# Kernel optimization log

Measured on AMD Instinct MI355X. Metric: run time of the kernel, lower is better.

The kernel has to match this reference:

```python
import jax, jax.numpy as jnp
import numpy as np

DIM = 192
TDIM = 192
HEADS = 6
WS = (2, 7, 7)
SS = (1, 3, 3)
MLP_HID = 4 * DIM
RANK = DIM // 8
EPS = 1e-6


def _rel_pos_index(ws):
    wd, wh, ww = ws
    coords = np.stack(np.meshgrid(np.arange(wd), np.arange(wh), np.arange(ww), indexing='ij'))
    cf = coords.reshape(3, -1)
    rel = (cf[:, :, None] - cf[:, None, :]).transpose(1, 2, 0).astype(np.int64)
    rel[..., 0] += wd - 1
    rel[..., 1] += wh - 1
    rel[..., 2] += ww - 1
    rel[..., 0] *= (2 * wh - 1) * (2 * ww - 1)
    rel[..., 1] *= (2 * ww - 1)
    return rel.sum(-1)  # (N, N)


def _window_partition(x, ws):
    B, D, H, W, C = x.shape
    x = x.reshape(B, D // ws[0], ws[0], H // ws[1], ws[1], W // ws[2], ws[2], C)
    return x.transpose(0, 1, 3, 5, 2, 4, 6, 7).reshape(-1, ws[0] * ws[1] * ws[2], C)


def _window_reverse(w, ws, B, D, H, W):
    x = w.reshape(B, D // ws[0], H // ws[1], W // ws[2], ws[0], ws[1], ws[2], -1)
    return x.transpose(0, 1, 4, 2, 5, 3, 6, 7).reshape(B, D, H, W, -1)


def _ln(x):
    m = x.mean(-1, keepdims=True)
    v = ((x - m) ** 2).mean(-1, keepdims=True)
    return (x - m) * jax.lax.rsqrt(v + EPS)


def _compute_mask_np(Dp, Hp, Wp, ws, ss):
    img = np.zeros((1, Dp, Hp, Wp, 1), dtype=np.float32)
    cnt = 0
    for d in (slice(0, -ws[0]), slice(-ws[0], -ss[0]), slice(-ss[0], None)):
        for h in (slice(0, -ws[1]), slice(-ws[1], -ss[1]), slice(-ss[1], None)):
            for w in (slice(0, -ws[2]), slice(-ws[2], -ss[2]), slice(-ss[2], None)):
                img[:, d, h, w, :] = cnt
                cnt += 1
    x = img.reshape(1, Dp // ws[0], ws[0], Hp // ws[1], ws[1], Wp // ws[2], ws[2], 1)
    mw = x.transpose(0, 1, 3, 5, 2, 4, 6, 7).reshape(-1, ws[0] * ws[1] * ws[2])
    am = mw[:, None, :] - mw[:, :, None]
    return np.where(am != 0, np.float32(-100.0), np.float32(0.0))


def setup_inputs() -> dict:
    key = jax.random.key(0)
    ks = jax.random.split(key, 16)
    B, D, H, W, C = 1, 16, 64, 128, DIM
    Dp = D + (-D) % WS[0]
    Hp = H + (-H) % WS[1]
    Wp = W + (-W) % WS[2]
    s = 0.02
    bias_tab = (2 * WS[0] - 1) * (2 * WS[1] - 1) * (2 * WS[2] - 1)
    return {
        'x': jax.random.normal(ks[0], (B, D, H, W, C), jnp.float32),
        'mask_matrix': jnp.asarray(_compute_mask_np(Dp, Hp, Wp, WS, SS)),
        't': jax.random.normal(ks[1], (B, TDIM), jnp.float32),
        'w_qkv': jax.random.normal(ks[2], (C, 3 * C), jnp.float32) * s,
        'b_qkv': jnp.zeros((3 * C,), jnp.float32),
        'rel_bias': jax.random.normal(ks[3], (bias_tab, HEADS), jnp.float32) * s,
        'w_proj': jax.random.normal(ks[4], (C, C), jnp.float32) * s,
        'b_proj': jnp.zeros((C,), jnp.float32),
        'w1': jax.random.normal(ks[5], (C, MLP_HID), jnp.float32) * s,
        'b1': jnp.zeros((MLP_HID,), jnp.float32),
        'w2': jax.random.normal(ks[6], (MLP_HID, C), jnp.float32) * s,
        'b2': jnp.zeros((C,), jnp.float32),
        'wa1': jax.random.normal(ks[7], (TDIM, RANK), jnp.float32) * s,
        'wa2': jax.random.normal(ks[8], (RANK, 6 * C), jnp.float32) * s,
        'ba2': jax.random.normal(ks[9], (6 * C,), jnp.float32) * s,
    }


def reference(x, mask_matrix, t, w_qkv, b_qkv, rel_bias, w_proj, b_proj, w1, b1, w2, b2, wa1, wa2, ba2):
    B, D, H, W, C = x.shape
    hd = C // HEADS
    # AdaLN modulation params
    mod = (jax.nn.silu(t) @ wa1) @ wa2 + ba2  # (B, 6C)
    sh_msa, sc_msa, g_msa, sh_mlp, sc_mlp, g_mlp = jnp.split(mod, 6, axis=1)

    def modulate(y, sh, sc):
        return y * (1 + sc[:, None, None, None, :]) + sh[:, None, None, None, :]

    shortcut = x
    y = modulate(_ln(x), sh_msa, sc_msa)
    # pad to window multiples
    pad_d, pad_h, pad_w = (-D) % WS[0], (-H) % WS[1], (-W) % WS[2]
    y = jnp.pad(y, ((0, 0), (0, pad_d), (0, pad_h), (0, pad_w), (0, 0)))
    Dp, Hp, Wp = D + pad_d, H + pad_h, W + pad_w
    # cyclic shift
    y = jnp.roll(y, (-SS[0], -SS[1], -SS[2]), axis=(1, 2, 3))
    xw = _window_partition(y, WS)  # (B*nW, N, C)
    N = xw.shape[1]
    qkv = (xw @ w_qkv + b_qkv).reshape(-1, N, 3, HEADS, hd)
    q, k, v = qkv[:, :, 0], qkv[:, :, 1], qkv[:, :, 2]
    scale = hd ** -0.5
    attn = jnp.einsum('bnhd,bmhd->bhnm', q * scale, k)  # (B*nW, H, N, N)
    rpi = _rel_pos_index(WS)
    bias = rel_bias[rpi.reshape(-1)].reshape(N, N, HEADS).transpose(2, 0, 1)
    attn = attn + bias[None]
    nW = mask_matrix.shape[0]
    attn = attn.reshape(B, nW, HEADS, N, N) + mask_matrix[None, :, None]
    attn = jax.nn.softmax(attn, axis=-1).reshape(-1, HEADS, N, N)
    out = jnp.einsum('bhnm,bmhd->bnhd', attn, v).reshape(-1, N, C)
    out = out @ w_proj + b_proj
    y = _window_reverse(out, WS, B, Dp, Hp, Wp)
    y = jnp.roll(y, (SS[0], SS[1], SS[2]), axis=(1, 2, 3))
    y = y[:, :D, :H, :W, :]
    x1 = shortcut + g_msa[:, None, None, None, :] * y
    y2 = modulate(_ln(x1), sh_mlp, sc_mlp)
    h = jax.nn.gelu(y2 @ w1 + b1, approximate=False) @ w2 + b2
    return x1 + g_mlp[:, None, None, None, :] * h
```

## Files before the change

### kernel.cpp

```cpp
#include <hip/hip_runtime.h>
#include <hip/hip_bf16.h>

typedef __bf16 bf16x8 __attribute__((ext_vector_type(8)));
typedef float  f32x4  __attribute__((ext_vector_type(4)));
typedef unsigned int u32x4 __attribute__((ext_vector_type(4)));

__device__ inline unsigned short f2bf(float f) {
    union { __hip_bfloat16 h; unsigned short u; } cv;
    cv.h = __float2bfloat16(f);
    return cv.u;
}

__device__ inline bf16x8 load8(const unsigned short* p) {
    uint2 lo = *(const uint2*)(p);
    uint2 hi = *(const uint2*)(p + 16);
    u32x4 v; v[0] = lo.x; v[1] = lo.y; v[2] = hi.x; v[3] = hi.y;
    return __builtin_bit_cast(bf16x8, v);
}

__device__ inline f32x4 mfma16(bf16x8 a, bf16x8 b, f32x4 c) {
    return __builtin_amdgcn_mfma_f32_16x16x32_bf16(a, b, c, 0, 0, 0);
}

__device__ inline bool winmapT(int gg, int& T) {
    int win = gg / 98, n = gg % 98;
    int wdi = win / 190, rem = win % 190, whi = rem / 19, wwi = rem % 19;
    int td = n / 49, th = (n / 7) % 7, tw = n % 7;
    int sd = (wdi * 2 + td + 1) & 15;
    int sh = whi * 7 + th + 3; if (sh >= 70) sh -= 70;
    int sw = wwi * 7 + tw + 3; if (sw >= 133) sw -= 133;
    if (sh < 64 && sw < 128) { T = (sd * 64 + sh) * 128 + sw; return true; }
    return false;
}

__global__ __launch_bounds__(256) void mod_k(const float* __restrict__ t,
    const float* __restrict__ wa1, const float* __restrict__ wa2,
    const float* __restrict__ ba2, float* __restrict__ mod)
{
    __shared__ float st[192];
    __shared__ float a[24];
    int tid = threadIdx.x;
    if (tid < 192) { float x = t[tid]; st[tid] = x / (1.f + __expf(-x)); }
    __syncthreads();
    if (tid < 24) {
        float s = 0.f;
        for (int c = 0; c < 192; ++c) s += st[c] * wa1[c * 24 + tid];
        a[tid] = s;
    }
    __syncthreads();
    for (int j = tid; j < 1152; j += 256) {
        float s = ba2[j];
        for (int r = 0; r < 24; ++r) s += a[r] * wa2[r * 1152 + j];
        mod[j] = s;
    }
}

__global__ __launch_bounds__(256) void prep_k(
    const float* __restrict__ wqkv, const float* __restrict__ wproj,
    const float* __restrict__ w1, const float* __restrict__ w2,
    const float* __restrict__ relb,
    unsigned short* __restrict__ wqkvT, unsigned short* __restrict__ wprojT,
    unsigned short* __restrict__ w1T, unsigned short* __restrict__ w2T,
    float* __restrict__ btab)
{
    int i = blockIdx.x * 256 + threadIdx.x;
    if (i < 110592) { int n = i / 192, k = i % 192; wqkvT[i] = f2bf(wqkv[k * 576 + n]); return; }
    i -= 110592;
    if (i < 36864)  { int n = i / 192, k = i % 192; wprojT[i] = f2bf(wproj[k * 192 + n]); return; }
    i -= 36864;
    if (i < 147456) { int n = i / 192, k = i % 192; w1T[i] = f2bf(w1[k * 768 + n]); return; }
    i -= 147456;
    if (i < 147456) { int n = i / 768, k = i % 768; w2T[i] = f2bf(w2[k * 192 + n]); return; }
    i -= 147456;
    if (i < 461952) {
        int mt = i / 57624, rem = i % 57624;
        int h = rem / 9604, rm2 = rem % 9604;
        int n = rm2 / 98, m = rm2 % 98;
        int tdn = n / 49, thn = (n / 7) % 7, twn = n % 7;
        int tdm = m / 49, thm = (m / 7) % 7, twm = m % 7;
        int idx = (tdn - tdm + 1) * 169 + (thn - thm + 6) * 13 + (twn - twm + 6);
        float b = relb[idx * 6 + h];
        int bd = mt & 1, bh = (mt >> 1) & 1, bw = (mt >> 2) & 1;
        int idn = (bd ? (tdn == 0 ? 1 : 2) : 0) * 9 + (bh ? (thn < 4 ? 1 : 2) : 0) * 3 + (bw ? (twn < 4 ? 1 : 2) : 0);
        int idm = (bd ? (tdm == 0 ? 1 : 2) : 0) * 9 + (bh ? (thm < 4 ? 1 : 2) : 0) * 3 + (bw ? (twm < 4 ? 1 : 2) : 0);
        btab[i] = b + ((idn != idm) ? -100.f : 0.f);
    }
}

__global__ __launch_bounds__(256) void stats_f32_k(const float* __restrict__ x,
    float* __restrict__ st)
{
    int tok = blockIdx.x * 4 + (threadIdx.x >> 6);
    int lane = threadIdx.x & 63;
    const float* p = x + (size_t)tok * 192;
    float a = p[lane], b = p[64 + lane], c = p[128 + lane];
    float s = a + b + c, q = a * a + b * b + c * c;
    for (int m = 32; m; m >>= 1) { s += __shfl_xor(s, m); q += __shfl_xor(q, m); }
    if (lane == 0) {
        float mean = s * (1.f / 192.f);
        float var  = q * (1.f / 192.f) - mean * mean;
        st[2 * tok] = mean;
        st[2 * tok + 1] = rsqrtf(var + 1e-6f);
    }
}

template<int FN, int STAGE, int EPI>
__global__ __launch_bounds__(256) void gemm_k(
    const unsigned short* __restrict__ A, const float* __restrict__ Af,
    const unsigned short* __restrict__ BT, const float* __restrict__ bias,
    unsigned short* __restrict__ outB, float* outF,
    const float* __restrict__ auxF, const float* __restrict__ stats,
    const float* __restrict__ mod, int row0, int M, int N, int K)
{
    constexpr int BN = FN * 32;
    __shared__ unsigned short As[128][44];
    __shared__ unsigned short Bs[BN][44];
    const int t = threadIdx.x;
    const int n0 = blockIdx.x * BN, m0 = blockIdx.y * 128;
    const int lr = t >> 2, lk = (t & 3) * 8;
    const int wid = t >> 6, lane = t & 63;
    const int lg = lane >> 4, l16 = lane & 15;
    const int wm = (wid >> 1) * 64, wn = (wid & 1) * (FN * 16);
    f32x4 acc[4][FN] = {};

    float mn[2] = {0.f, 0.f}, rs[2] = {0.f, 0.f};
    size_t sbase[2] = {0, 0};
    bool va[2] = {false, false};
    #pragma unroll
    for (int rr = 0; rr < 2; ++rr) {
        int g = m0 + lr + rr * 64;
        if (STAGE == 1) {
            int T;
            if (g < M && winmapT(row0 + g, T)) {
                va[rr] = true; sbase[rr] = (size_t)T * 192;
                mn[rr] = stats[2 * T]; rs[rr] = stats[2 * T + 1];
            }
        } else if (STAGE == 2) {
            int tok = row0 + g;
            sbase[rr] = (size_t)tok * 192;
            mn[rr] = stats[2 * tok]; rs[rr] = stats[2 * tok + 1];
        }
    }

    for (int kk = 0; kk < K; kk += 32) {
        #pragma unroll
        for (int rr = 0; rr < 2; ++rr) {
            int r = lr + rr * 64;
            int g = m0 + r;
            uint4 w = make_uint4(0u, 0u, 0u, 0u);
            if (STAGE == 0) {
                if (g < M) w = *(const uint4*)(A + (size_t)g * K + kk + lk);
            } else if (STAGE == 1) {
                if (va[rr]) {
                    float4 xa = *(const float4*)(Af + sbase[rr] + kk + lk);
                    float4 xb = *(const float4*)(Af + sbase[rr] + kk + lk + 4);
                    float xs[8] = {xa.x, xa.y, xa.z, xa.w, xb.x, xb.y, xb.z, xb.w};
                    unsigned short o[8];
                    #pragma unroll
                    for (int j = 0; j < 8; ++j) {
                        int c = kk + lk + j;
                        o[j] = f2bf((xs[j] - mn[rr]) * rs[rr] * (1.f + mod[192 + c]) + mod[c]);
                    }
                    w = make_uint4((unsigned)o[0] | ((unsigned)o[1] << 16), (unsigned)o[2] | ((unsigned)o[3] << 16),
                                   (unsigned)o[4] | ((unsigned)o[5] << 16), (unsigned)o[6] | ((unsigned)o[7] << 16));
                }
            } else {
                float4 xa = *(const float4*)(Af + sbase[rr] + kk + lk);
                float4 xb = *(const float4*)(Af + sbase[rr] + kk + lk + 4);
                float xs[8] = {xa.x, xa.y, xa.z, xa.w, xb.x, xb.y, xb.z, xb.w};
                unsigned short o[8];
                #pragma unroll
                for (int j = 0; j < 8; ++j) {
                    int c = kk + lk + j;
                    o[j] = f2bf((xs[j] - mn[rr]) * rs[rr] * (1.f + mod[768 + c]) + mod[576 + c]);
                }
                w = make_uint4((unsigned)o[0] | ((unsigned)o[1] << 16), (unsigned)o[2] | ((unsigned)o[3] << 16),
                               (unsigned)o[4] | ((unsigned)o[5] << 16), (unsigned)o[6] | ((unsigned)o[7] << 16));
            }
            *(uint2*)(&As[r][lk])     = make_uint2(w.x, w.y);
            *(uint2*)(&As[r][lk + 4]) = make_uint2(w.z, w.w);
        }
        #pragma unroll
        for (int rr = 0; rr < BN / 64; ++rr) {
            int r = lr + rr * 64;
            int gn = n0 + r;
            uint4 w = make_uint4(0u, 0u, 0u, 0u);
            if (gn < N) w = *(const uint4*)(BT + (size_t)gn * K + kk + lk);
            *(uint2*)(&Bs[r][lk])     = make_uint2(w.x, w.y);
            *(uint2*)(&Bs[r][lk + 4]) = make_uint2(w.z, w.w);
        }
        __syncthreads();
        bf16x8 af[4], bv[FN];
        #pragma unroll
        for (int i = 0; i < 4; ++i) af[i] = load8(&As[wm + i * 16 + l16][4 * lg]);
        #pragma unroll
        for (int j = 0; j < FN; ++j) bv[j] = load8(&Bs[wn + j * 16 + l16][4 * lg]);
        #pragma unroll
        for (int i = 0; i < 4; ++i)
        #pragma unroll
        for (int j = 0; j < FN; ++j)
            acc[i][j] = mfma16(af[i], bv[j], acc[i][j]);
        __syncthreads();
    }

    #pragma unroll
    for (int i = 0; i < 4; ++i)
    #pragma unroll
    for (int j = 0; j < FN; ++j) {
        int gcol = n0 + wn + j * 16 + l16;
        if (gcol >= N) continue;
        float b = bias[gcol];
        #pragma unroll
        for (int e = 0; e < 4; ++e) {
            int grow = m0 + wm + i * 16 + lg * 4 + e;
            if (grow >= M) continue;
            float v = acc[i][j][e] + b;
            if (EPI == 0) {
                outB[(size_t)grow * N + gcol] = f2bf(v);
            } else if (EPI == 1) {
                float gl = 0.5f * v * (1.f + erff(v * 0.70710678118654752f));
                outB[(size_t)grow * N + gcol] = f2bf(gl);
            } else if (EPI == 2) {
                int T;
                if (winmapT(row0 + grow, T)) {
                    size_t idx = (size_t)T * 192 + gcol;
                    outF[idx] = auxF[idx] + mod[384 + gcol] * v;
                }
            } else {
                size_t idx = (size_t)(row0 + grow) * 192 + gcol;
                outF[idx] = outF[idx] + mod[960 + gcol] * v;
            }
        }
    }
}

__global__ __launch_bounds__(256) void attn_k(
    const unsigned short* __restrict__ qkv, const float* __restrict__ btab,
    unsigned short* __restrict__ out)
{
    __shared__ __align__(16) char smem[40320];
    unsigned short* Qs  = (unsigned short*)smem;
    unsigned short* Ks  = (unsigned short*)(smem + 9856);
    unsigned short* Pbf = (unsigned short*)smem;
    unsigned short* VT  = (unsigned short*)(smem + 31360);

    const int blk = blockIdx.x;
    const int win = blk / 6, h = blk % 6;
    const int t = threadIdx.x;
    const int wid = t >> 6, lg = (t >> 4) & 3, l16 = t & 15;
    const size_t rb = (size_t)win * 98;

    const int wdi = win / 190, remw = win % 190, whi = remw / 19, wwi = remw % 19;
    const int mt = (wdi == 7 ? 1 : 0) | (whi == 9 ? 2 : 0) | (wwi == 18 ? 4 : 0);
    const float* bt = btab + (size_t)(mt * 6 + h) * 9604;

    for (int i = t; i < 98 * 4; i += 256) {
        int r = i >> 2, cg = (i & 3) * 8;
        uint4 q = *(const uint4*)(qkv + (rb + r) * 576 + h * 32 + cg);
        uint4 k = *(const uint4*)(qkv + (rb + r) * 576 + 192 + h * 32 + cg);
        *(uint2*)(Qs + r * 44 + cg)     = make_uint2(q.x, q.y);
        *(uint2*)(Qs + r * 44 + cg + 4) = make_uint2(q.z, q.w);
        *(uint2*)(Ks + r * 44 + cg)     = make_uint2(k.x, k.y);
        *(uint2*)(Ks + r * 44 + cg + 4) = make_uint2(k.z, k.w);
    }
    for (int i = t; i < 14 * 32; i += 256) {
        int r = 98 + (i >> 5), c = i & 31;
        Qs[r * 44 + c] = 0; Ks[r * 44 + c] = 0;
    }
    for (int i = t; i < 32 * 42; i += 256) { int c = i / 42, m = 98 + i % 42; VT[c * 140 + m] = 0; }
    for (int i = t; i < 98 * 32; i += 256) {
        int m = i >> 5, c = i & 31;
        VT[c * 140 + m] = qkv[(rb + m) * 576 + 384 + h * 32 + c];
    }
    __syncthreads();

    f32x4 acc[2][7];
    {
        bf16x8 kb[7];
        #pragma unroll
        for (int fn = 0; fn < 7; ++fn) kb[fn] = load8(Ks + (fn * 16 + l16) * 44 + 4 * lg);
        #pragma unroll
        for (int fi = 0; fi < 2; ++fi) {
            int fm = wid + fi * 4;
            if (fm < 7) {
                bf16x8 qa = load8(Qs + (fm * 16 + l16) * 44 + 4 * lg);
                #pragma unroll
                for (int fn = 0; fn < 7; ++fn) {
                    f32x4 z = {};
                    acc[fi][fn] = mfma16(qa, kb[fn], z);
                }
            }
        }
    }
    __syncthreads();

    const float SCALE = 0.17677669529663687f;
    float rinv[2][4];
    #pragma unroll
    for (int fi = 0; fi < 2; ++fi) {
        int fm = wid + fi * 4;
        if (fm < 7) {
            #pragma unroll
            for (int e = 0; e < 4; ++e) {
                int r = fm * 16 + lg * 4 + e;
                float mx = -1e30f;
                #pragma unroll
                for (int fn = 0; fn < 7; ++fn) {
                    int c = fn * 16 + l16;
                    float s = -1e30f;
                    if (r < 98 && c < 98) s = fmaf(acc[fi][fn][e], SCALE, bt[r * 98 + c]);
                    acc[fi][fn][e] = s;
                    mx = fmaxf(mx, s);
                }
                #pragma unroll
                for (int m = 1; m < 16; m <<= 1) mx = fmaxf(mx, __shfl_xor(mx, m));
                float sum = 0.f;
                #pragma unroll
                for (int fn = 0; fn < 7; ++fn) {
                    float p = __expf(acc[fi][fn][e] - mx);
                    acc[fi][fn][e] = p;
                    sum += p;
                }
                #pragma unroll
                for (int m = 1; m < 16; m <<= 1) sum += __shfl_xor(sum, m);
                rinv[fi][e] = 1.f / sum;
            }
            #pragma unroll
            for (int fn = 0; fn < 7; ++fn) {
                int c = fn * 16 + l16;
                #pragma unroll
                for (int e = 0; e < 4; ++e) {
                    int r = fm * 16 + lg * 4 + e;
                    float val = (r < 98 && c < 98) ? acc[fi][fn][e] : 0.f;
                    Pbf[r * 140 + c] = f2bf(val);
                }
            }
        }
    }
    for (int i = t; i < 112 * 8; i += 256) {
        int r = i >> 3, c = 112 + (i & 7) * 2;
        *(unsigned int*)(Pbf + r * 140 + c) = 0u;
    }
    __syncthreads();

    #pragma unroll
    for (int fi = 0; fi < 2; ++fi) {
        int fm = wid + fi * 4;
        if (fm < 7) {
            bf16x8 sa[4];
            #pragma unroll
            for (int ks = 0; ks < 4; ++ks)
                sa[ks] = load8(Pbf + (fm * 16 + l16) * 140 + ks * 32 + 4 * lg);
            #pragma unroll
            for (int fn = 0; fn < 2; ++fn) {
                f32x4 o = {};
                #pragma unroll
                for (int ks = 0; ks < 4; ++ks) {
                    bf16x8 vb = load8(VT + (fn * 16 + l16) * 140 + ks * 32 + 4 * lg);
                    o = mfma16(sa[ks], vb, o);
                }
                #pragma unroll
                for (int e = 0; e < 4; ++e) {
                    int r = fm * 16 + lg * 4 + e;
                    if (r < 98) {
                        out[(rb + r) * 192 + h * 32 + fn * 16 + l16] = f2bf(o[e] * rinv[fi][e]);
                    }
                }
            }
        }
    }
}

extern "C" void kernel_launch(void* const* d_in, const int* in_sizes, int n_in,
                              void* d_out, int out_size, void* d_ws, size_t ws_size,
                              hipStream_t stream)
{
    const float* x      = (const float*)d_in[0];
    const float* tvec   = (const float*)d_in[2];
    const float* w_qkv  = (const float*)d_in[3];
    const float* b_qkv  = (const float*)d_in[4];
    const float* relb   = (const float*)d_in[5];
    const float* w_proj = (const float*)d_in[6];
    const float* b_proj = (const float*)d_in[7];
    const float* w1     = (const float*)d_in[8];
    const float* b1     = (const float*)d_in[9];
    const float* w2     = (const float*)d_in[10];
    const float* b2     = (const float*)d_in[11];
    const float* wa1    = (const float*)d_in[12];
    const float* wa2    = (const float*)d_in[13];
    const float* ba2    = (const float*)d_in[14];

    char* ws = (char*)d_ws;
    float*          mod    = (float*)ws;
    float*          stats1 = (float*)(ws + 4608);
    float*          stats2 = (float*)(ws + 1053184);
    unsigned short* wqkvT  = (unsigned short*)(ws + 2101760);
    unsigned short* wprojT = (unsigned short*)(ws + 2322944);
    unsigned short* w1T    = (unsigned short*)(ws + 2396672);
    unsigned short* w2T    = (unsigned short*)(ws + 2691584);
    float*          btab   = (float*)(ws + 2986496);
    unsigned short* qkvb   = (unsigned short*)(ws + 4834304);
    unsigned short* h      = (unsigned short*)(ws + 4834304);
    unsigned short* attn_c = (unsigned short*)(ws + 176436224);
    float*          dout   = (float*)d_out;

    mod_k<<<1, 256, 0, stream>>>(tvec, wa1, wa2, ba2, mod);
    prep_k<<<3533, 256, 0, stream>>>(w_qkv, w_proj, w1, w2, relb, wqkvT, wprojT, w1T, w2T, btab);
    stats_f32_k<<<32768, 256, 0, stream>>>(x, stats1);

    gemm_k<4, 1, 0><<<dim3(5, 1164), 256, 0, stream>>>(
        nullptr, x, wqkvT, b_qkv, qkvb, nullptr, nullptr, stats1, mod, 0, 148960, 576, 192);
    attn_k<<<9120, 256, 0, stream>>>(qkvb, btab, attn_c);
    gemm_k<2, 0, 2><<<dim3(3, 1164), 256, 0, stream>>>(
        attn_c, nullptr, wprojT, b_proj, nullptr, dout, x, nullptr, mod, 0, 148960, 192, 192);

    stats_f32_k<<<32768, 256, 0, stream>>>(dout, stats2);

    gemm_k<4, 2, 1><<<dim3(6, 1024), 256, 0, stream>>>(
        nullptr, dout, w1T, b1, h, nullptr, nullptr, stats2, mod, 0, 131072, 768, 192);
    gemm_k<2, 0, 3><<<dim3(3, 1024), 256, 0, stream>>>(
        h, nullptr, w2T, b2, nullptr, dout, nullptr, nullptr, mod, 0, 131072, 192, 768);
}
```

Measured before the change: 1.041 ms.

## Store attention bias/mask table in bf16 fragment-order layout and prefetch V into registers

The combined relative-position bias and shift mask table is now precomputed in bf16, laid out in MFMA fragment order with padding baked in as -1e30. Each lane can then fetch its bias values with a few 16-byte loads instead of many scattered fp32 loads and bounds checks. V is loaded into registers at kernel start and transposed into shared memory after the QK MFMA, so the global load latency overlaps the first matmul. The LDS row stride changes from 140 to 142, and rounding the bias to bf16 adds a small accuracy loss.

After: 1.020 ms. -2.0%, faster.

```diff
diff --git a/kernel.cpp b/kernel.cpp
--- a/kernel.cpp
+++ b/kernel.cpp
@@ -9,6 +9,9 @@
     union { __hip_bfloat16 h; unsigned short u; } cv;
     cv.h = __float2bfloat16(f);
     return cv.u;
+}
+__device__ inline float bf2f(unsigned short u) {
+    union { unsigned int i; float f; } c; c.i = ((unsigned int)u) << 16; return c.f;
 }
 
 __device__ inline bf16x8 load8(const unsigned short* p) {
@@ -61,7 +64,7 @@
     const float* __restrict__ relb,
     unsigned short* __restrict__ wqkvT, unsigned short* __restrict__ wprojT,
     unsigned short* __restrict__ w1T, unsigned short* __restrict__ w2T,
-    float* __restrict__ btab)
+    unsigned short* __restrict__ btabF)
 {
     int i = blockIdx.x * 256 + threadIdx.x;
     if (i < 110592) { int n = i / 192, k = i % 192; wqkvT[i] = f2bf(wqkv[k * 576 + n]); return; }
@@ -72,18 +75,27 @@
     i -= 147456;
     if (i < 147456) { int n = i / 768, k = i % 768; w2T[i] = f2bf(w2[k * 192 + n]); return; }
     i -= 147456;
-    if (i < 461952) {
-        int mt = i / 57624, rem = i % 57624;
-        int h = rem / 9604, rm2 = rem % 9604;
-        int n = rm2 / 98, m = rm2 % 98;
-        int tdn = n / 49, thn = (n / 7) % 7, twn = n % 7;
-        int tdm = m / 49, thm = (m / 7) % 7, twm = m % 7;
-        int idx = (tdn - tdm + 1) * 169 + (thn - thm + 6) * 13 + (twn - twm + 6);
-        float b = relb[idx * 6 + h];
-        int bd = mt & 1, bh = (mt >> 1) & 1, bw = (mt >> 2) & 1;
-        int idn = (bd ? (tdn == 0 ? 1 : 2) : 0) * 9 + (bh ? (thn < 4 ? 1 : 2) : 0) * 3 + (bw ? (twn < 4 ? 1 : 2) : 0);
-        int idm = (bd ? (tdm == 0 ? 1 : 2) : 0) * 9 + (bh ? (thm < 4 ? 1 : 2) : 0) * 3 + (bw ? (twm < 4 ? 1 : 2) : 0);
-        btab[i] = b + ((idn != idm) ? -100.f : 0.f);
+    if (i < 688128) {
+        int mt = i / 86016, r1 = i % 86016;
+        int h  = r1 / 14336, r2 = r1 % 14336;
+        int fm = r2 / 2048,  r3 = r2 % 2048;
+        int le = r3 / 128,   r4 = r3 % 128;
+        int l16 = r4 / 8,    fn = r4 % 8;
+        int r = fm * 16 + le, c = fn * 16 + l16;
+        float val;
+        if (fn == 7 || r >= 98 || c >= 98) {
+            val = -1e30f;
+        } else {
+            int tdn = r / 49, thn = (r / 7) % 7, twn = r % 7;
+            int tdm = c / 49, thm = (c / 7) % 7, twm = c % 7;
+            int idx = (tdn - tdm + 1) * 169 + (thn - thm + 6) * 13 + (twn - twm + 6);
+            float b = relb[idx * 6 + h];
+            int bd = mt & 1, bh = (mt >> 1) & 1, bw = (mt >> 2) & 1;
+            int idn = (bd ? (tdn == 0 ? 1 : 2) : 0) * 9 + (bh ? (thn < 4 ? 1 : 2) : 0) * 3 + (bw ? (twn < 4 ? 1 : 2) : 0);
+            int idm = (bd ? (tdm == 0 ? 1 : 2) : 0) * 9 + (bh ? (thm < 4 ? 1 : 2) : 0) * 3 + (bw ? (twm < 4 ? 1 : 2) : 0);
+            val = b + ((idn != idm) ? -100.f : 0.f);
+        }
+        btabF[i] = f2bf(val);
     }
 }
 
@@ -235,14 +247,14 @@
 }
 
 __global__ __launch_bounds__(256) void attn_k(
-    const unsigned short* __restrict__ qkv, const float* __restrict__ btab,
+    const unsigned short* __restrict__ qkv, const unsigned short* __restrict__ btabF,
     unsigned short* __restrict__ out)
 {
-    __shared__ __align__(16) char smem[40320];
+    __shared__ __align__(16) char smem[40896];
     unsigned short* Qs  = (unsigned short*)smem;
     unsigned short* Ks  = (unsigned short*)(smem + 9856);
     unsigned short* Pbf = (unsigned short*)smem;
-    unsigned short* VT  = (unsigned short*)(smem + 31360);
+    unsigned short* VT  = (unsigned short*)(smem + 31808);
 
     const int blk = blockIdx.x;
     const int win = blk / 6, h = blk % 6;
@@ -252,7 +264,12 @@
 
     const int wdi = win / 190, remw = win % 190, whi = remw / 19, wwi = remw % 19;
     const int mt = (wdi == 7 ? 1 : 0) | (whi == 9 ? 2 : 0) | (wwi == 18 ? 4 : 0);
-    const float* bt = btab + (size_t)(mt * 6 + h) * 9604;
+    const unsigned short* btF = btabF + (size_t)(mt * 6 + h) * 14336;
+
+    uint4 vreg[2];
+    const int vi0 = t, vi1 = t + 256;
+    if (vi0 < 392) vreg[0] = *(const uint4*)(qkv + (rb + (vi0 >> 2)) * 576 + 384 + h * 32 + (vi0 & 3) * 8);
+    if (vi1 < 392) vreg[1] = *(const uint4*)(qkv + (rb + (vi1 >> 2)) * 576 + 384 + h * 32 + (vi1 & 3) * 8);
 
     for (int i = t; i < 98 * 4; i += 256) {
         int r = i >> 2, cg = (i & 3) * 8;
@@ -267,11 +284,6 @@
         int r = 98 + (i >> 5), c = i & 31;
         Qs[r * 44 + c] = 0; Ks[r * 44 + c] = 0;
     }
-    for (int i = t; i < 32 * 42; i += 256) { int c = i / 42, m = 98 + i % 42; VT[c * 140 + m] = 0; }
-    for (int i = t; i < 98 * 32; i += 256) {
-        int m = i >> 5, c = i & 31;
-        VT[c * 140 + m] = qkv[(rb + m) * 576 + 384 + h * 32 + c];
-    }
     __syncthreads();
 
     f32x4 acc[2][7];
@@ -294,6 +306,35 @@
     }
     __syncthreads();
 
+    uint4 btreg[2][4];
+    #pragma unroll
+    for (int fi = 0; fi < 2; ++fi) {
+        int fm = wid + fi * 4;
+        int fmc = (fm < 7) ? fm : 0;
+        #pragma unroll
+        for (int e = 0; e < 4; ++e)
+            btreg[fi][e] = *(const uint4*)(btF + fmc * 2048 + (lg * 4 + e) * 128 + l16 * 8);
+    }
+    {
+        if (vi0 < 392) {
+            int m = vi0 >> 2, c0 = (vi0 & 3) * 8;
+            const unsigned short* vp = (const unsigned short*)&vreg[0];
+            #pragma unroll
+            for (int j = 0; j < 8; ++j) VT[(c0 + j) * 142 + m] = vp[j];
+        }
+        if (vi1 < 392) {
+            int m = vi1 >> 2, c0 = (vi1 & 3) * 8;
+            const unsigned short* vp = (const unsigned short*)&vreg[1];
+            #pragma unroll
+            for (int j = 0; j < 8; ++j) VT[(c0 + j) * 142 + m] = vp[j];
+        }
+    }
+    for (int i = t; i < 32 * 30; i += 256) { int c = i / 30, m = 98 + i % 30; VT[c * 142 + m] = 0; }
+    for (int i = t; i < 112 * 8; i += 256) {
+        int r = i >> 3, cc = 112 + (i & 7) * 2;
+        *(unsigned int*)(Pbf + r * 142 + cc) = 0u;
+    }
+
     const float SCALE = 0.17677669529663687f;
     float rinv[2][4];
     #pragma unroll
@@ -302,13 +343,12 @@
         if (fm < 7) {
             #pragma unroll
             for (int e = 0; e < 4; ++e) {
-                int r = fm * 16 + lg * 4 + e;
+                const unsigned int bw[4] = {btreg[fi][e].x, btreg[fi][e].y, btreg[fi][e].z, btreg[fi][e].w};
                 float mx = -1e30f;
                 #pragma unroll
                 for (int fn = 0; fn < 7; ++fn) {
-                    int c = fn * 16 + l16;
-                    float s = -1e30f;
-                    if (r < 98 && c < 98) s = fmaf(acc[fi][fn][e], SCALE, bt[r * 98 + c]);
+                    unsigned short bu = (unsigned short)(bw[fn >> 1] >> ((fn & 1) * 16));
+                    float s = fmaf(acc[fi][fn][e], SCALE, bf2f(bu));
                     acc[fi][fn][e] = s;
                     mx = fmaxf(mx, s);
                 }
@@ -331,15 +371,10 @@
                 #pragma unroll
                 for (int e = 0; e < 4; ++e) {
                     int r = fm * 16 + lg * 4 + e;
-                    float val = (r < 98 && c < 98) ? acc[fi][fn][e] : 0.f;
-                    Pbf[r * 140 + c] = f2bf(val);
-                }
-            }
-        }
-    }
-    for (int i = t; i < 112 * 8; i += 256) {
-        int r = i >> 3, c = 112 + (i & 7) * 2;
-        *(unsigned int*)(Pbf + r * 140 + c) = 0u;
+                    Pbf[r * 142 + c] = f2bf(acc[fi][fn][e]);
+                }
+            }
+        }
     }
     __syncthreads();
 
@@ -350,13 +385,13 @@
             bf16x8 sa[4];
             #pragma unroll
             for (int ks = 0; ks < 4; ++ks)
-                sa[ks] = load8(Pbf + (fm * 16 + l16) * 140 + ks * 32 + 4 * lg);
+                sa[ks] = load8(Pbf + (fm * 16 + l16) * 142 + ks * 32 + 4 * lg);
             #pragma unroll
             for (int fn = 0; fn < 2; ++fn) {
                 f32x4 o = {};
                 #pragma unroll
                 for (int ks = 0; ks < 4; ++ks) {
-                    bf16x8 vb = load8(VT + (fn * 16 + l16) * 140 + ks * 32 + 4 * lg);
+                    bf16x8 vb = load8(VT + (fn * 16 + l16) * 142 + ks * 32 + 4 * lg);
                     o = mfma16(sa[ks], vb, o);
                 }
                 #pragma unroll
@@ -398,19 +433,19 @@
     unsigned short* wprojT = (unsigned short*)(ws + 2322944);
     unsigned short* w1T    = (unsigned short*)(ws + 2396672);
     unsigned short* w2T    = (unsigned short*)(ws + 2691584);
-    float*          btab   = (float*)(ws + 2986496);
+    unsigned short* btabF  = (unsigned short*)(ws + 2986496);
     unsigned short* qkvb   = (unsigned short*)(ws + 4834304);
     unsigned short* h      = (unsigned short*)(ws + 4834304);
     unsigned short* attn_c = (unsigned short*)(ws + 176436224);
     float*          dout   = (float*)d_out;
 
     mod_k<<<1, 256, 0, stream>>>(tvec, wa1, wa2, ba2, mod);
-    prep_k<<<3533, 256, 0, stream>>>(w_qkv, w_proj, w1, w2, relb, wqkvT, wprojT, w1T, w2T, btab);
+    prep_k<<<4416, 256, 0, stream>>>(w_qkv, w_proj, w1, w2, relb, wqkvT, wprojT, w1T, w2T, btabF);
     stats_f32_k<<<32768, 256, 0, stream>>>(x, stats1);
 
     gemm_k<4, 1, 0><<<dim3(5, 1164), 256, 0, stream>>>(
         nullptr, x, wqkvT, b_qkv, qkvb, nullptr, nullptr, stats1, mod, 0, 148960, 576, 192);
-    attn_k<<<9120, 256, 0, stream>>>(qkvb, btab, attn_c);
+    attn_k<<<9120, 256, 0, stream>>>(qkvb, btabF, attn_c);
     gemm_k<2, 0, 2><<<dim3(3, 1164), 256, 0, stream>>>(
         attn_c, nullptr, wprojT, b_proj, nullptr, dout, x, nullptr, mod, 0, 148960, 192, 192);
 
```
